# Optimization experiments

Measured on AMD Instinct MI355X. Metric: run time of the kernel, lower is better.

Reference implementation:

```python
import jax, jax.numpy as jnp
import numpy as np

B, C, H, W = 64, 3, 256, 256
K = 2  # multi_n_num
EPS_NORM = 1e-8
EPS_DEN = 1e-7
SCALE = 0.01


def setup_inputs() -> dict:
    key = jax.random.key(0)
    ka, kp, kn, kj = jax.random.split(key, 4)
    a = jax.random.normal(ka, (B, C, H, W), dtype=jnp.float32)
    p = jax.random.normal(kp, (B, C, H, W), dtype=jnp.float32)
    n = jax.random.normal(kn, (B, C, H, W), dtype=jnp.float32)
    # sample_with_j(B, 2, i) -> [i, random j != i]
    ar = jnp.arange(B, dtype=jnp.int64)
    off = jax.random.randint(kj, (B,), 1, B)  # offset in [1, B) guarantees j != i
    neg_idx = jnp.stack([ar, (ar + off) % B], axis=1).astype(jnp.int64)  # [B, K]
    return {"a": a, "p": p, "n": n, "neg_idx": neg_idx}


def _fft_norm(x):
    # torch.fft.fft2 over last two dims -> complex, same rank as x
    f = jnp.fft.fft2(x, axes=(-2, -1))  # [B, C, H, W] complex64
    # torch.norm(f, p=2, dim=1, keepdim=True) on complex = sqrt(sum |f|^2 over C)
    nrm = jnp.sqrt(jnp.sum(jnp.abs(f) ** 2, axis=1, keepdims=True))
    return f / (nrm + EPS_NORM) * SCALE


def reference(a, p, n, neg_idx):
    af = _fft_norm(a)
    pf = _fft_norm(p)
    nf = _fft_norm(n)
    # L1Loss on complex tensors = mean |diff| (complex magnitude)
    d_ap = jnp.mean(jnp.abs(af - pf), axis=(1, 2, 3))  # [B]
    n_sel = nf[neg_idx]  # [B, K, C, H, W]
    d_an = jnp.mean(jnp.abs(af[:, None] - n_sel), axis=(2, 3, 4))  # [B, K]
    contrastive = jnp.sum(d_ap[:, None] / (d_an + EPS_DEN))
    return contrastive / (K * B)
```

## Files before the change

kernel.cpp:

```cpp
#include <hip/hip_runtime.h>
#include <hip/hip_fp16.h>

#define B_ 64
#define SW_ 132
#define SIMG_ (256 * SW_)
#define TIMG_ (3 * SIMG_)
#define TELEMS_ ((size_t)B_ * TIMG_)
#define SST_ 257

typedef unsigned u32;

__device__ __forceinline__ u32 h2add(u32 a, u32 b) {
  __half2 r = __hadd2(__builtin_bit_cast(__half2, a), __builtin_bit_cast(__half2, b));
  return __builtin_bit_cast(u32, r);
}
__device__ __forceinline__ u32 h2sub(u32 a, u32 b) {
  __half2 r = __hsub2(__builtin_bit_cast(__half2, a), __builtin_bit_cast(__half2, b));
  return __builtin_bit_cast(u32, r);
}
__device__ __forceinline__ u32 h2mul(u32 a, u32 b) {
  __half2 r = __hmul2(__builtin_bit_cast(__half2, a), __builtin_bit_cast(__half2, b));
  return __builtin_bit_cast(u32, r);
}
__device__ __forceinline__ u32 h2fma(u32 a, u32 b, u32 c) {
  __half2 r = __hfma2(__builtin_bit_cast(__half2, a), __builtin_bit_cast(__half2, b),
                      __builtin_bit_cast(__half2, c));
  return __builtin_bit_cast(u32, r);
}
__device__ __forceinline__ u32 rot16(u32 u) { return (u >> 16) | (u << 16); }
#define NEG_HI_ 0x80000000u
#define NEG_LO_ 0x00008000u
#define HALF2C_ 0x38003800u

__device__ __forceinline__ u32 cmulh(u32 x, u32 tr, u32 ti) {
  u32 m = h2mul(rot16(x), ti);
  return h2fma(x, tr, m ^ NEG_LO_);
}

__device__ __forceinline__ u32 f2u(float2 v) {
  __half2 h = __float22half2_rn(v);
  return __builtin_bit_cast(u32, h);
}
__device__ __forceinline__ float2 u2f(u32 u) {
  return __half22float2(__builtin_bit_cast(__half2, u));
}
__device__ __forceinline__ float2 cmulf(float2 a, float2 b) {
  return make_float2(a.x * b.x - a.y * b.y, a.x * b.y + a.y * b.x);
}

__device__ __forceinline__ void bfly4h(u32 x[4], const u32* twr, const u32* twi, bool tw) {
  u32 a = h2add(x[0], x[2]);
  u32 b = h2sub(x[0], x[2]);
  u32 c = h2add(x[1], x[3]);
  u32 d = h2sub(x[1], x[3]);
  u32 e = rot16(d);
  u32 y1 = h2add(b, e ^ NEG_HI_);
  u32 y2 = h2sub(a, c);
  u32 y3 = h2add(b, e ^ NEG_LO_);
  x[0] = h2add(a, c);
  if (tw) { y1 = cmulh(y1, twr[0], twi[0]); y2 = cmulh(y2, twr[1], twi[1]);
            y3 = cmulh(y3, twr[2], twi[2]); }
  x[1] = y1; x[2] = y2; x[3] = y3;
}

__device__ __forceinline__ void swap16(u32& A, u32& B) {
  asm("v_permlane16_swap_b32 %0, %1" : "+v"(A), "+v"(B));
}
__device__ __forceinline__ void swap32(u32& A, u32& B) {
  asm("v_permlane32_swap_b32 %0, %1" : "+v"(A), "+v"(B));
}
template <int BIT>
__device__ __forceinline__ void xsel(u32& A, u32& B, int r) {
  bool hi = (r >> BIT) & 1;
  int send = hi ? (int)A : (int)B;
  int got;
  if constexpr (BIT == 0)
    got = __builtin_amdgcn_update_dpp(0, send, 0xB1, 0xF, 0xF, false);
  else if constexpr (BIT == 1)
    got = __builtin_amdgcn_update_dpp(0, send, 0x4E, 0xF, 0xF, false);
  else if constexpr (BIT == 2)
    got = __builtin_amdgcn_ds_swizzle(send, 0x101F);
  else
    got = __builtin_amdgcn_ds_swizzle(send, 0x201F);
  if (hi) A = (u32)got; else B = (u32)got;
}
__device__ __forceinline__ void xdig45(u32 u[4]) {
  swap16(u[0], u[1]);
  swap16(u[2], u[3]);
  swap32(u[0], u[2]);
  swap32(u[1], u[3]);
}
template <int BIT>
__device__ __forceinline__ void xdig(u32 u[4], int r) {
  xsel<BIT>(u[0], u[1], r);
  xsel<BIT>(u[2], u[3], r);
  xsel<BIT + 1>(u[0], u[2], r);
  xsel<BIT + 1>(u[1], u[3], r);
}

template <int NF>
__device__ __forceinline__ void fft256h(u32 (&u)[NF][4], int r,
                                        const u32 twr[9], const u32 twi[9]) {
#pragma unroll
  for (int f = 0; f < NF; ++f) bfly4h(u[f], twr + 0, twi + 0, true);
#pragma unroll
  for (int f = 0; f < NF; ++f) xdig45(u[f]);
#pragma unroll
  for (int f = 0; f < NF; ++f) bfly4h(u[f], twr + 3, twi + 3, true);
#pragma unroll
  for (int f = 0; f < NF; ++f) xdig<2>(u[f], r);
#pragma unroll
  for (int f = 0; f < NF; ++f) bfly4h(u[f], twr + 6, twi + 6, true);
#pragma unroll
  for (int f = 0; f < NF; ++f) xdig<0>(u[f], r);
#pragma unroll
  for (int f = 0; f < NF; ++f) bfly4h(u[f], twr, twi, false);
}

__device__ __forceinline__ void tw_init_h(u32 twr[9], u32 twi[9], int r) {
  float2 t[9];
  float s, c;
  __sincosf(-6.283185307179586f * (float)r / 256.0f, &s, &c);
  t[0] = make_float2(c, s); t[1] = cmulf(t[0], t[0]); t[2] = cmulf(t[1], t[0]);
  __sincosf(-6.283185307179586f * (float)(r & 15) / 64.0f, &s, &c);
  t[3] = make_float2(c, s); t[4] = cmulf(t[3], t[3]); t[5] = cmulf(t[4], t[3]);
  __sincosf(-6.283185307179586f * (float)(r & 3) / 16.0f, &s, &c);
  t[6] = make_float2(c, s); t[7] = cmulf(t[6], t[6]); t[8] = cmulf(t[7], t[6]);
#pragma unroll
  for (int i = 0; i < 9; ++i) {
    u32 hr = (u32)__half_as_ushort(__float2half_rn(t[i].x));
    u32 hi = (u32)__half_as_ushort(__float2half_rn(t[i].y));
    twr[i] = hr | (hr << 16);
    twi[i] = hi | (hi << 16);
  }
}

__global__ __launch_bounds__(1024, 8) void fft2_fused(const float* __restrict__ a,
                                                      const float* __restrict__ p,
                                                      const float* __restrict__ n,
                                                      unsigned* __restrict__ outbase,
                                                      float* __restrict__ acc) {
  __shared__ u32 S[65 * SST_];

  int tid = threadIdx.x;
  int wv = tid >> 6;
  int r = tid & 63;
  int tensor = blockIdx.x / 192;
  int plane = blockIdx.x % 192;
  const float* in = (tensor == 0 ? a : (tensor == 1 ? p : n)) + (size_t)plane * 65536;
  unsigned* outp = outbase + (size_t)tensor * TELEMS_ + (size_t)plane * SIMG_;

  if (blockIdx.x == 0 && tid < 192) acc[tid] = 0.0f;

  u32 twr[9], twi[9];
  tw_init_h(twr, twi, r);
  int m = ((r & 3) << 4) | (((r >> 2) & 3) << 2) | (r >> 4);
  int mp = (64 - m) & 63;
  int rp = ((mp >> 4) & 3) | (((mp >> 2) & 3) << 2) | ((mp & 3) << 4);

  u32 ba[8], bb[8];

  {
    u32 u[8][4];
#pragma unroll
    for (int f = 0; f < 8; ++f) {
      int q = wv + 16 * f;
      const float* rw = in + (size_t)(2 * q) * 256;
#pragma unroll
      for (int j = 0; j < 4; ++j)
        u[f][j] = f2u(make_float2(rw[r + 64 * j], rw[256 + r + 64 * j]));
    }
    fft256h<8>(u, r, twr, twi);
#pragma unroll
    for (int f = 0; f < 8; ++f) {
      int q = wv + 16 * f;
      u32 m0 = (u32)__shfl((int)u[f][0], rp, 64);
      u32 m2 = (u32)__shfl((int)u[f][2], rp, 64);
      u32 m3 = (u32)__shfl((int)u[f][3], rp, 64);
      u32 Zk0 = u[f][0];
      u32 Zk1 = u[f][1];
      u32 Zm0 = (m == 0) ? m0 : m3;
      u32 Zm1 = (m == 0) ? m3 : m2;
      u32 Aa = h2mul(HALF2C_, h2add(Zk0, Zm0 ^ NEG_HI_));
      u32 Ab = h2mul(HALF2C_, h2add(rot16(Zm0), rot16(Zk0) ^ NEG_HI_));
      ba[f]  = h2mul(HALF2C_, h2add(Zk1, Zm1 ^ NEG_HI_));
      bb[f]  = h2mul(HALF2C_, h2add(rot16(Zm1), rot16(Zk1) ^ NEG_HI_));
      S[m * SST_ + 2 * q]     = Aa;
      S[m * SST_ + 2 * q + 1] = Ab;
      if (r == 0) {
        S[64 * SST_ + 2 * q]     = u[f][2] & 0xFFFFu;
        S[64 * SST_ + 2 * q + 1] = u[f][2] >> 16;
      }
    }
  }

  __syncthreads();

  u32 uA[4][4];
#pragma unroll
  for (int f = 0; f < 4; ++f) {
    const u32* row = S + (size_t)(wv + 16 * f) * SST_;
#pragma unroll
    for (int j = 0; j < 4; ++j) uA[f][j] = row[r + 64 * j];
  }

  __syncthreads();

#pragma unroll
  for (int f = 0; f < 8; ++f) {
    int q = wv + 16 * f;
    S[m * SST_ + 2 * q]     = ba[f];
    S[m * SST_ + 2 * q + 1] = bb[f];
  }

  fft256h<4>(uA, r, twr, twi);
#pragma unroll
  for (int f = 0; f < 4; ++f) {
    int c = wv + 16 * f;
    *(uint4*)(outp + (size_t)c * 256 + 4 * r) =
        make_uint4(uA[f][0], uA[f][1], uA[f][2], uA[f][3]);
  }
  if (wv >= 13) {
    int c = 129 + (wv - 13);
    *(uint4*)(outp + (size_t)c * 256 + 4 * r) = make_uint4(0, 0, 0, 0);
  }

  __syncthreads();

  {
    u32 uB[4][4];
#pragma unroll
    for (int f = 0; f < 4; ++f) {
      const u32* row = S + (size_t)(wv + 16 * f) * SST_;
#pragma unroll
      for (int j = 0; j < 4; ++j) uB[f][j] = row[r + 64 * j];
    }
    fft256h<4>(uB, r, twr, twi);
#pragma unroll
    for (int f = 0; f < 4; ++f) {
      int c = 64 + wv + 16 * f;
      *(uint4*)(outp + (size_t)c * 256 + 4 * r) =
          make_uint4(uB[f][0], uB[f][1], uB[f][2], uB[f][3]);
    }
  }
  if (wv == 0) {
    u32 u1[1][4];
    const u32* srow = S + 64 * SST_;
#pragma unroll
    for (int j = 0; j < 4; ++j) u1[0][j] = srow[r + 64 * j];
    fft256h<1>(u1, r, twr, twi);
    *(uint4*)(outp + (size_t)128 * 256 + 4 * r) =
        make_uint4(u1[0][0], u1[0][1], u1[0][2], u1[0][3]);
  }
}

__device__ __forceinline__ float cab2(float2 v) { return v.x * v.x + v.y * v.y; }
__device__ __forceinline__ float fsqrt_(float x) { return __builtin_amdgcn_sqrtf(x); }
__device__ __forceinline__ float frcp_(float x) { return __builtin_amdgcn_rcpf(x); }

__global__ __launch_bounds__(256) void dist_kernel(const unsigned* __restrict__ af,
                                                   const unsigned* __restrict__ pf,
                                                   const unsigned* __restrict__ nf,
                                                   const int* __restrict__ neg,
                                                   float* __restrict__ acc) {
  int b = blockIdx.y;
  int j = (neg[1] == 0) ? (int)((const long long*)neg)[b * 2 + 1] : neg[b * 2 + 1];
  size_t ab = (size_t)b * TIMG_;
  size_t jb = (size_t)j * TIMG_;
  int t4 = blockIdx.x * 256 + threadIdx.x;
  int flat0 = t4 * 4;
  int k2 = flat0 >> 8;
  float w = (k2 == 0 || k2 >= 128) ? 1.0f : 2.0f;

  unsigned A[3][4], P[3][4], N[3][4], M[3][4];
#pragma unroll
  for (int ch = 0; ch < 3; ++ch) {
    uint4 t;
    t = *(const uint4*)(af + ab + ch * SIMG_ + flat0); A[ch][0]=t.x; A[ch][1]=t.y; A[ch][2]=t.z; A[ch][3]=t.w;
    t = *(const uint4*)(pf + ab + ch * SIMG_ + flat0); P[ch][0]=t.x; P[ch][1]=t.y; P[ch][2]=t.z; P[ch][3]=t.w;
    t = *(const uint4*)(nf + ab + ch * SIMG_ + flat0); N[ch][0]=t.x; N[ch][1]=t.y; N[ch][2]=t.z; N[ch][3]=t.w;
    t = *(const uint4*)(nf + jb + ch * SIMG_ + flat0); M[ch][0]=t.x; M[ch][1]=t.y; M[ch][2]=t.z; M[ch][3]=t.w;
  }
  float s_ap = 0.0f, s_a0 = 0.0f, s_a1 = 0.0f;
#pragma unroll
  for (int e = 0; e < 4; ++e) {
    float2 a0 = u2f(A[0][e]), a1 = u2f(A[1][e]), a2 = u2f(A[2][e]);
    float2 p0 = u2f(P[0][e]), p1 = u2f(P[1][e]), p2 = u2f(P[2][e]);
    float2 n0 = u2f(N[0][e]), n1 = u2f(N[1][e]), n2 = u2f(N[2][e]);
    float2 m0 = u2f(M[0][e]), m1 = u2f(M[1][e]), m2 = u2f(M[2][e]);
    float sa = 0.01f * frcp_(fsqrt_(cab2(a0) + cab2(a1) + cab2(a2)) + 1e-8f);
    float sp = 0.01f * frcp_(fsqrt_(cab2(p0) + cab2(p1) + cab2(p2)) + 1e-8f);
    float sn = 0.01f * frcp_(fsqrt_(cab2(n0) + cab2(n1) + cab2(n2)) + 1e-8f);
    float sm = 0.01f * frcp_(fsqrt_(cab2(m0) + cab2(m1) + cab2(m2)) + 1e-8f);
    float dx, dy;
    dx = a0.x * sa - p0.x * sp; dy = a0.y * sa - p0.y * sp; s_ap += fsqrt_(dx * dx + dy * dy);
    dx = a1.x * sa - p1.x * sp; dy = a1.y * sa - p1.y * sp; s_ap += fsqrt_(dx * dx + dy * dy);
    dx = a2.x * sa - p2.x * sp; dy = a2.y * sa - p2.y * sp; s_ap += fsqrt_(dx * dx + dy * dy);
    dx = a0.x * sa - n0.x * sn; dy = a0.y * sa - n0.y * sn; s_a0 += fsqrt_(dx * dx + dy * dy);
    dx = a1.x * sa - n1.x * sn; dy = a1.y * sa - n1.y * sn; s_a0 += fsqrt_(dx * dx + dy * dy);
    dx = a2.x * sa - n2.x * sn; dy = a2.y * sa - n2.y * sn; s_a0 += fsqrt_(dx * dx + dy * dy);
    dx = a0.x * sa - m0.x * sm; dy = a0.y * sa - m0.y * sm; s_a1 += fsqrt_(dx * dx + dy * dy);
    dx = a1.x * sa - m1.x * sm; dy = a1.y * sa - m1.y * sm; s_a1 += fsqrt_(dx * dx + dy * dy);
    dx = a2.x * sa - m2.x * sm; dy = a2.y * sa - m2.y * sm; s_a1 += fsqrt_(dx * dx + dy * dy);
  }
  s_ap *= w; s_a0 *= w; s_a1 *= w;
#pragma unroll
  for (int off = 32; off > 0; off >>= 1) {
    s_ap += __shfl_down(s_ap, off);
    s_a0 += __shfl_down(s_a0, off);
    s_a1 += __shfl_down(s_a1, off);
  }
  __shared__ float red[3][4];
  int lane = threadIdx.x & 63, wid = threadIdx.x >> 6;
  if (lane == 0) { red[0][wid] = s_ap; red[1][wid] = s_a0; red[2][wid] = s_a1; }
  __syncthreads();
  if (threadIdx.x == 0) {
    atomicAdd(&acc[b * 3 + 0], red[0][0] + red[0][1] + red[0][2] + red[0][3]);
    atomicAdd(&acc[b * 3 + 1], red[1][0] + red[1][1] + red[1][2] + red[1][3]);
    atomicAdd(&acc[b * 3 + 2], red[2][0] + red[2][1] + red[2][2] + red[2][3]);
  }
}

__global__ void final_kernel(const float* __restrict__ acc, float* __restrict__ out) {
  int b = threadIdx.x;
  const float inv = 1.0f / 196608.0f;
  float dap = acc[b * 3 + 0] * inv;
  float da0 = acc[b * 3 + 1] * inv;
  float da1 = acc[b * 3 + 2] * inv;
  float term = dap / (da0 + 1e-7f) + dap / (da1 + 1e-7f);
#pragma unroll
  for (int off = 32; off > 0; off >>= 1) term += __shfl_down(term, off);
  if (b == 0) out[0] = term * (1.0f / 128.0f);
}

extern "C" void kernel_launch(void* const* d_in, const int* in_sizes, int n_in,
                              void* d_out, int out_size, void* d_ws, size_t ws_size,
                              hipStream_t stream) {
  const float* a = (const float*)d_in[0];
  const float* p = (const float*)d_in[1];
  const float* n = (const float*)d_in[2];
  const int* neg = (const int*)d_in[3];
  float* out = (float*)d_out;

  unsigned* base = (unsigned*)d_ws;
  float* acc = (float*)(base + 3 * TELEMS_);

  fft2_fused<<<576, 1024, 0, stream>>>(a, p, n, base, acc);
  dist_kernel<<<dim3(33, 64), 256, 0, stream>>>(base, base + TELEMS_,
                                                base + 2 * TELEMS_, neg, acc);
  final_kernel<<<1, 64, 0, stream>>>(acc, out);
}
```

Baseline: 261.8 us.

## Split each FFT plane across two blocks, recomputing row FFT per half

Each 2D FFT plane is now processed by two blocks: both compute the full row FFT, then each writes only its half of the unpacked spectrum to shared memory and performs the column FFTs for that half. This doubles the grid size to improve load balance and latency hiding and removes a register-held buffer and one barrier. The cost is duplicated global input reads and a duplicated row-FFT pass.

```diff
diff --git a/kernel.cpp b/kernel.cpp
--- a/kernel.cpp
+++ b/kernel.cpp
@@ -145,8 +145,10 @@
   int tid = threadIdx.x;
   int wv = tid >> 6;
   int r = tid & 63;
-  int tensor = blockIdx.x / 192;
-  int plane = blockIdx.x % 192;
+  int pb = blockIdx.x >> 1;
+  int half = blockIdx.x & 1;
+  int tensor = pb / 192;
+  int plane = pb % 192;
   const float* in = (tensor == 0 ? a : (tensor == 1 ? p : n)) + (size_t)plane * 65536;
   unsigned* outp = outbase + (size_t)tensor * TELEMS_ + (size_t)plane * SIMG_;
 
@@ -158,8 +160,6 @@
   int mp = (64 - m) & 63;
   int rp = ((mp >> 4) & 3) | (((mp >> 2) & 3) << 2) | ((mp & 3) << 4);
 
-  u32 ba[8], bb[8];
-
   {
     u32 u[8][4];
 #pragma unroll
@@ -171,86 +171,69 @@
         u[f][j] = f2u(make_float2(rw[r + 64 * j], rw[256 + r + 64 * j]));
     }
     fft256h<8>(u, r, twr, twi);
-#pragma unroll
-    for (int f = 0; f < 8; ++f) {
-      int q = wv + 16 * f;
-      u32 m0 = (u32)__shfl((int)u[f][0], rp, 64);
-      u32 m2 = (u32)__shfl((int)u[f][2], rp, 64);
-      u32 m3 = (u32)__shfl((int)u[f][3], rp, 64);
-      u32 Zk0 = u[f][0];
-      u32 Zk1 = u[f][1];
-      u32 Zm0 = (m == 0) ? m0 : m3;
-      u32 Zm1 = (m == 0) ? m3 : m2;
-      u32 Aa = h2mul(HALF2C_, h2add(Zk0, Zm0 ^ NEG_HI_));
-      u32 Ab = h2mul(HALF2C_, h2add(rot16(Zm0), rot16(Zk0) ^ NEG_HI_));
-      ba[f]  = h2mul(HALF2C_, h2add(Zk1, Zm1 ^ NEG_HI_));
-      bb[f]  = h2mul(HALF2C_, h2add(rot16(Zm1), rot16(Zk1) ^ NEG_HI_));
-      S[m * SST_ + 2 * q]     = Aa;
-      S[m * SST_ + 2 * q + 1] = Ab;
-      if (r == 0) {
-        S[64 * SST_ + 2 * q]     = u[f][2] & 0xFFFFu;
-        S[64 * SST_ + 2 * q + 1] = u[f][2] >> 16;
+    if (half == 0) {
+#pragma unroll
+      for (int f = 0; f < 8; ++f) {
+        int q = wv + 16 * f;
+        u32 m0 = (u32)__shfl((int)u[f][0], rp, 64);
+        u32 m3 = (u32)__shfl((int)u[f][3], rp, 64);
+        u32 Zk0 = u[f][0];
+        u32 Zm0 = (m == 0) ? m0 : m3;
+        S[m * SST_ + 2 * q]     = h2mul(HALF2C_, h2add(Zk0, Zm0 ^ NEG_HI_));
+        S[m * SST_ + 2 * q + 1] = h2mul(HALF2C_, h2add(rot16(Zm0), rot16(Zk0) ^ NEG_HI_));
       }
+    } else {
+#pragma unroll
+      for (int f = 0; f < 8; ++f) {
+        int q = wv + 16 * f;
+        u32 m2 = (u32)__shfl((int)u[f][2], rp, 64);
+        u32 m3 = (u32)__shfl((int)u[f][3], rp, 64);
+        u32 Zk1 = u[f][1];
+        u32 Zm1 = (m == 0) ? m3 : m2;
+        S[m * SST_ + 2 * q]     = h2mul(HALF2C_, h2add(Zk1, Zm1 ^ NEG_HI_));
+        S[m * SST_ + 2 * q + 1] = h2mul(HALF2C_, h2add(rot16(Zm1), rot16(Zk1) ^ NEG_HI_));
+        if (r == 0) {
+          S[64 * SST_ + 2 * q]     = u[f][2] & 0xFFFFu;
+          S[64 * SST_ + 2 * q + 1] = u[f][2] >> 16;
+        }
+      }
     }
   }
 
   __syncthreads();
 
-  u32 uA[4][4];
-#pragma unroll
-  for (int f = 0; f < 4; ++f) {
-    const u32* row = S + (size_t)(wv + 16 * f) * SST_;
-#pragma unroll
-    for (int j = 0; j < 4; ++j) uA[f][j] = row[r + 64 * j];
-  }
-
-  __syncthreads();
-
-#pragma unroll
-  for (int f = 0; f < 8; ++f) {
-    int q = wv + 16 * f;
-    S[m * SST_ + 2 * q]     = ba[f];
-    S[m * SST_ + 2 * q + 1] = bb[f];
-  }
-
-  fft256h<4>(uA, r, twr, twi);
-#pragma unroll
-  for (int f = 0; f < 4; ++f) {
-    int c = wv + 16 * f;
-    *(uint4*)(outp + (size_t)c * 256 + 4 * r) =
-        make_uint4(uA[f][0], uA[f][1], uA[f][2], uA[f][3]);
-  }
-  if (wv >= 13) {
-    int c = 129 + (wv - 13);
-    *(uint4*)(outp + (size_t)c * 256 + 4 * r) = make_uint4(0, 0, 0, 0);
-  }
-
-  __syncthreads();
-
   {
-    u32 uB[4][4];
+    u32 u[4][4];
 #pragma unroll
     for (int f = 0; f < 4; ++f) {
       const u32* row = S + (size_t)(wv + 16 * f) * SST_;
 #pragma unroll
-      for (int j = 0; j < 4; ++j) uB[f][j] = row[r + 64 * j];
-    }
-    fft256h<4>(uB, r, twr, twi);
+      for (int j = 0; j < 4; ++j) u[f][j] = row[r + 64 * j];
+    }
+    fft256h<4>(u, r, twr, twi);
+    int kbase = half * 64;
 #pragma unroll
     for (int f = 0; f < 4; ++f) {
-      int c = 64 + wv + 16 * f;
+      int c = kbase + wv + 16 * f;
       *(uint4*)(outp + (size_t)c * 256 + 4 * r) =
-          make_uint4(uB[f][0], uB[f][1], uB[f][2], uB[f][3]);
-    }
-  }
-  if (wv == 0) {
-    u32 u1[1][4];
-    const u32* srow = S + 64 * SST_;
-#pragma unroll
-    for (int j = 0; j < 4; ++j) u1[0][j] = srow[r + 64 * j];
-    fft256h<1>(u1, r, twr, twi);
-    *(uint4*)(outp + (size_t)128 * 256 + 4 * r) =
-        make_uint4(u1[0][0], u1[0][1], u1[0][2], u1[0][3]);
+          make_uint4(u[f][0], u[f][1], u[f][2], u[f][3]);
+    }
+  }
+  if (half == 1) {
+    if (wv == 0) {
+      u32 u1[1][4];
+      const u32* srow = S + 64 * SST_;
+#pragma unroll
+      for (int j = 0; j < 4; ++j) u1[0][j] = srow[r + 64 * j];
+      fft256h<1>(u1, r, twr, twi);
+      *(uint4*)(outp + (size_t)128 * 256 + 4 * r) =
+          make_uint4(u1[0][0], u1[0][1], u1[0][2], u1[0][3]);
+    }
+  } else {
+    if (wv >= 13) {
+      int c = 129 + (wv - 13);
+      *(uint4*)(outp + (size_t)c * 256 + 4 * r) = make_uint4(0, 0, 0, 0);
+    }
   }
 }
 
@@ -345,7 +328,7 @@
   unsigned* base = (unsigned*)d_ws;
   float* acc = (float*)(base + 3 * TELEMS_);
 
-  fft2_fused<<<576, 1024, 0, stream>>>(a, p, n, base, acc);
+  fft2_fused<<<1152, 1024, 0, stream>>>(a, p, n, base, acc);
   dist_kernel<<<dim3(33, 64), 256, 0, stream>>>(base, base + TELEMS_,
                                                 base + 2 * TELEMS_, neg, acc);
   final_kernel<<<1, 64, 0, stream>>>(acc, out);
```

Result: slower. 285.7 us (+9.1%).
